# Kernel tuning notes

Hardware: AMD Instinct MI355X
Metric: run time of the kernel (lower is better)

## Reference

```python
import jax, jax.numpy as jnp
import numpy as np

B, S, D_MODEL = 2, 2048, 1024
NUM_HEADS = 16
D_HEAD = D_MODEL // NUM_HEADS
THETA = 10000.0


def setup_inputs() -> dict:
    key = jax.random.key(0)
    ks = jax.random.split(key, 5)
    std = float(np.sqrt(2.0 / (D_MODEL + D_MODEL)))
    return {
        "x": jax.random.normal(ks[0], (B, S, D_MODEL), dtype=jnp.float32),
        "wq": jax.random.normal(ks[1], (D_MODEL, D_MODEL), dtype=jnp.float32) * std,
        "wk": jax.random.normal(ks[2], (D_MODEL, D_MODEL), dtype=jnp.float32) * std,
        "wv": jax.random.normal(ks[3], (D_MODEL, D_MODEL), dtype=jnp.float32) * std,
        "wo": jax.random.normal(ks[4], (D_MODEL, D_MODEL), dtype=jnp.float32) * std,
    }


def _apply_rope(x):
    # x: [b, h, s, d]; interleaved even/odd RoPE rotation
    d = x.shape[-1]
    s = x.shape[-2]
    inv_freq = 1.0 / (THETA ** (jnp.arange(0, d, 2, dtype=x.dtype) / d))  # [d/2]
    pos = jnp.arange(s, dtype=x.dtype)
    freqs = pos[:, None] * inv_freq[None, :]  # [s, d/2]
    cos, sin = jnp.cos(freqs), jnp.sin(freqs)
    x_even = x[..., 0::2]
    x_odd = x[..., 1::2]
    rot_even = x_even * cos - x_odd * sin
    rot_odd = x_even * sin + x_odd * cos
    # interleave back: stack pairs on a new trailing axis then flatten
    return jnp.stack([rot_even, rot_odd], axis=-1).reshape(x.shape)


def reference(x, wq, wk, wv, wo):
    b, s, _ = x.shape
    # Linear applies weight [d_out, d_in] as x @ W^T
    q = jnp.einsum('bsd,ed->bse', x, wq)
    k = jnp.einsum('bsd,ed->bse', x, wk)
    v = jnp.einsum('bsd,ed->bse', x, wv)
    # [b, s, h*dh] -> [b, h, s, dh]
    q = q.reshape(b, s, NUM_HEADS, D_HEAD).transpose(0, 2, 1, 3)
    k = k.reshape(b, s, NUM_HEADS, D_HEAD).transpose(0, 2, 1, 3)
    v = v.reshape(b, s, NUM_HEADS, D_HEAD).transpose(0, 2, 1, 3)
    q = _apply_rope(q)
    k = _apply_rope(k)
    scores = jnp.einsum('bhqd,bhkd->bhqk', q, k) / jnp.sqrt(jnp.asarray(D_HEAD, x.dtype))
    causal = jnp.tril(jnp.ones((s, s), dtype=bool))  # allowed positions
    scores = jnp.where(causal, scores, -jnp.inf)
    attn = jax.nn.softmax(scores, axis=-1)
    out = jnp.einsum('bhqk,bhkd->bhqd', attn, v)
    out = out.transpose(0, 2, 1, 3).reshape(b, s, NUM_HEADS * D_HEAD)
    return jnp.einsum('bsd,ed->bse', out, wo)
```

## Files before the change

### kernel.cpp

```cpp
#include <hip/hip_runtime.h>
#include <stdint.h>

typedef unsigned short u16;
typedef __attribute__((ext_vector_type(8))) short bf16x8;
typedef __attribute__((ext_vector_type(4))) short bf16x4;
typedef __attribute__((ext_vector_type(4))) float f32x4;
typedef __attribute__((ext_vector_type(4))) unsigned short u16x4;
typedef __attribute__((ext_vector_type(2))) unsigned u32x2;

#define S_ 2048
#define E_ 1024
#define QSCALE 0.18033688011112042f

__device__ __forceinline__ u16 f2bf(float f) {
  union { float f; unsigned u; } v; v.f = f;
  unsigned u = v.u;
  unsigned r = (u + 0x7FFFu + ((u >> 16) & 1u)) >> 16;
  return (u16)r;
}
__device__ __forceinline__ float bf2f(u16 h) {
  union { unsigned u; float f; } v; v.u = ((unsigned)h) << 16;
  return v.f;
}
__device__ __forceinline__ unsigned cvtpk(float a, float b) {
  unsigned r;
  asm("v_cvt_pk_bf16_f32 %0, %1, %2" : "=v"(r) : "v"(a), "v"(b));
  return r;
}
__device__ __forceinline__ bf16x4 pk4(float a, float b, float c, float d) {
  union { u32x2 u; bf16x4 v; } U;
  U.u[0] = cvtpk(a, b);
  U.u[1] = cvtpk(c, d);
  return U.v;
}

typedef __attribute__((address_space(3))) void lds_void;
__device__ __forceinline__ unsigned lds_off(void* p) {
  return (unsigned)(unsigned long long)(lds_void*)p;
}
__device__ __forceinline__ void glds16(const u16* g, u16* l) {
  __builtin_amdgcn_global_load_lds(
      (const __attribute__((address_space(1))) void*)g,
      (__attribute__((address_space(3))) void*)l, 16, 0, 0);
}

__global__ void k_cast5(const float* __restrict__ x,
                        const float* __restrict__ wq, const float* __restrict__ wk,
                        const float* __restrict__ wv, const float* __restrict__ wo,
                        u16* __restrict__ xb, u16* __restrict__ wqb, u16* __restrict__ wkb,
                        u16* __restrict__ wvb, u16* __restrict__ wob) {
  int i = blockIdx.x * blockDim.x + threadIdx.x;
  const float* src; u16* dst; int off;
  if (i < 1048576) { src = x; dst = xb; off = i; }
  else {
    int j = i - 1048576;
    int w = j >> 18; off = j & 262143;
    src = (w == 0) ? wq : (w == 1) ? wk : (w == 2) ? wv : wo;
    dst = (w == 0) ? wqb : (w == 1) ? wkb : (w == 2) ? wvb : wob;
  }
  float4 v = *((const float4*)src + off);
  u16x4 o;
  o.x = f2bf(v.x); o.y = f2bf(v.y); o.z = f2bf(v.z); o.w = f2bf(v.w);
  *((u16x4*)dst + off) = o;
}

__global__ __launch_bounds__(256) void k_gemm(
    const u16* __restrict__ A,
    const u16* __restrict__ W0, const u16* __restrict__ W1, const u16* __restrict__ W2,
    void* O0, void* O1, void* O2, int outF32)
{
  __shared__ __align__(16) u16 As[2][128 * 32];
  __shared__ __align__(16) u16 Ws[2][128 * 32];
  int tid = threadIdx.x;
  int wid = tid >> 6, lane = tid & 63;
  int lg = lane >> 4, lr = lane & 15;
  int wsel = blockIdx.y >> 3, nb = blockIdx.y & 7;
  const u16* W = (wsel == 0) ? W0 : ((wsel == 1) ? W1 : W2);
  void* O = (wsel == 0) ? O0 : ((wsel == 1) ? O1 : O2);
  int m0 = blockIdx.x * 128;
  int n0 = nb * 128;
  int wr = wid >> 1, wc = wid & 1;

  f32x4 acc[4][4];
#pragma unroll
  for (int m = 0; m < 4; m++)
#pragma unroll
    for (int n = 0; n < 4; n++) acc[m][n] = (f32x4){0.f, 0.f, 0.f, 0.f};

  int srow = tid >> 2;
  int schunk = (tid & 3) ^ ((tid >> 3) & 3);
  const u16* ag = A + (size_t)(m0 + srow) * 1024 + schunk * 8;
  const u16* wg = W + (size_t)(n0 + srow) * 1024 + schunk * 8;

  int buf = 0;
  glds16(ag, &As[0][tid * 8]);
  glds16(ag + 65536, &As[0][tid * 8 + 2048]);
  glds16(wg, &Ws[0][tid * 8]);
  glds16(wg + 65536, &Ws[0][tid * 8 + 2048]);
  __syncthreads();

  for (int kt = 0; kt < 1024; kt += 32) {
    if (kt + 32 < 1024) {
      glds16(ag + kt + 32, &As[buf ^ 1][tid * 8]);
      glds16(ag + kt + 32 + 65536, &As[buf ^ 1][tid * 8 + 2048]);
      glds16(wg + kt + 32, &Ws[buf ^ 1][tid * 8]);
      glds16(wg + kt + 32 + 65536, &Ws[buf ^ 1][tid * 8 + 2048]);
    }
    bf16x8 af[4], wf[4];
#pragma unroll
    for (int m = 0; m < 4; m++) {
      int row = wr * 64 + m * 16 + lr;
      af[m] = *(const bf16x8*)&As[buf][row * 32 + ((lg ^ ((row >> 1) & 3)) * 8)];
    }
#pragma unroll
    for (int n = 0; n < 4; n++) {
      int row = wc * 64 + n * 16 + lr;
      wf[n] = *(const bf16x8*)&Ws[buf][row * 32 + ((lg ^ ((row >> 1) & 3)) * 8)];
    }
    __builtin_amdgcn_s_setprio(1);
#pragma unroll
    for (int m = 0; m < 4; m++)
#pragma unroll
      for (int n = 0; n < 4; n++)
        acc[m][n] = __builtin_amdgcn_mfma_f32_16x16x32_bf16(af[m], wf[n], acc[m][n], 0, 0, 0);
    __builtin_amdgcn_s_setprio(0);
    __syncthreads();
    buf ^= 1;
  }

#pragma unroll
  for (int m = 0; m < 4; m++) {
    int gr = m0 + wr * 64 + m * 16 + lg * 4;
#pragma unroll
    for (int n = 0; n < 4; n++) {
      int gc = n0 + wc * 64 + n * 16 + lr;
#pragma unroll
      for (int r = 0; r < 4; r++) {
        if (outF32) ((float*)O)[(size_t)(gr + r) * 1024 + gc] = acc[m][n][r];
        else ((u16*)O)[(size_t)(gr + r) * 1024 + gc] = f2bf(acc[m][n][r]);
      }
    }
  }
}

__global__ void k_rope(u16* __restrict__ Q, u16* __restrict__ K) {
  int idx = blockIdx.x * blockDim.x + threadIdx.x;
  int p = idx & 511;
  int srow = idx >> 9;
  int s = srow & (S_ - 1);
  int i = p & 31;
  float ang = (float)s * exp2f(-0.415241012f * (float)i);
  float sn, c;
  __sincosf(ang, &sn, &c);
  unsigned* qp = (unsigned*)Q + idx;
  unsigned qv = *qp;
  float e = bf2f((u16)(qv & 0xffff)), o = bf2f((u16)(qv >> 16));
  float re = (e * c - o * sn) * QSCALE, ro = (e * sn + o * c) * QSCALE;
  *qp = cvtpk(re, ro);
  unsigned* kp = (unsigned*)K + idx;
  unsigned kv = *kp;
  e = bf2f((u16)(kv & 0xffff)); o = bf2f((u16)(kv >> 16));
  re = e * c - o * sn; ro = e * sn + o * c;
  *kp = cvtpk(re, ro);
}

__global__ __launch_bounds__(256) void k_attn(
    const u16* __restrict__ Q, const u16* __restrict__ K,
    const u16* __restrict__ V, u16* __restrict__ AO)
{
  __shared__ __align__(16) u16 Ks[64 * 64];
  __shared__ __align__(16) u16 Vs[64 * 64];
  int tid = threadIdx.x;
  int wid = tid >> 6, lane = tid & 63;
  int lg = lane >> 4, lr = lane & 15;
  int bh = blockIdx.x;
  int qb = 31 - (int)blockIdx.y;
  int q0 = qb * 64 + wid * 16;
  size_t base = (size_t)(bh >> 4) * (2048u * 1024u) + (size_t)(bh & 15) * 64;

  const u16* qrow = Q + base + (size_t)(q0 + lr) * 1024 + lg * 8;
  bf16x8 qf0 = *(const bf16x8*)(qrow);
  bf16x8 qf1 = *(const bf16x8*)(qrow + 32);

  int srow = tid >> 3;
  int sch = tid & 7;
  const u16* kg = K + base + (size_t)srow * 1024 + sch * 8;
  const u16* vg = V + base + (size_t)srow * 1024 + sch * 8;
  int kwb0 = ((srow)*128 + sch * 16) ^ ((srow & 7) << 4);
  int kwb1 = ((srow + 32) * 128 + sch * 16) ^ ((srow & 7) << 4);
  int vwi0 = (srow >> 4) * 1024 + (sch >> 1) * 256 + (srow & 15) * 16 + (sch & 1) * 8;
  int vwi1 = ((srow + 32) >> 4) * 1024 + (sch >> 1) * 256 + (srow & 15) * 16 + (sch & 1) * 8;

  bf16x8 kr0 = *(const bf16x8*)(kg);
  bf16x8 kr1 = *(const bf16x8*)(kg + 32 * 1024);
  bf16x8 vr0 = *(const bf16x8*)(vg);
  bf16x8 vr1 = *(const bf16x8*)(vg + 32 * 1024);
  const u16* kgp = kg + 64 * 1024;
  const u16* vgp = vg + 64 * 1024;

  float m = -1e30f, lsum = 0.f;
  f32x4 o[4];
#pragma unroll
  for (int c = 0; c < 4; c++) o[c] = (f32x4){0.f, 0.f, 0.f, 0.f};

  int qg = q0 + lr;
  int ntile = qb + 1;
  unsigned vrd = lds_off(Vs) + (unsigned)(lane * 8);

  for (int t = 0; t < ntile; ++t) {
    __syncthreads();
    *(bf16x8*)((char*)Ks + kwb0) = kr0;
    *(bf16x8*)((char*)Ks + kwb1) = kr1;
    *(bf16x8*)(&Vs[vwi0]) = vr0;
    *(bf16x8*)(&Vs[vwi1]) = vr1;
    __syncthreads();
    if (t + 1 < ntile) {
      kr0 = *(const bf16x8*)(kgp);
      kr1 = *(const bf16x8*)(kgp + 32 * 1024);
      vr0 = *(const bf16x8*)(vgp);
      vr1 = *(const bf16x8*)(vgp + 32 * 1024);
      kgp += 64 * 1024;
      vgp += 64 * 1024;
    }
    f32x4 sv[4];
    int kv0 = t * 64;
    __builtin_amdgcn_s_setprio(1);
#pragma unroll
    for (int sub = 0; sub < 4; ++sub) {
      int row = sub * 16 + lr;
      int swz = (row & 7) << 4;
      bf16x8 kf0 = *(const bf16x8*)((const char*)Ks + ((row * 128 + lg * 16) ^ swz));
      bf16x8 kf1 = *(const bf16x8*)((const char*)Ks + ((row * 128 + 64 + lg * 16) ^ swz));
      f32x4 z = (f32x4){0.f, 0.f, 0.f, 0.f};
      z = __builtin_amdgcn_mfma_f32_16x16x32_bf16(kf0, qf0, z, 0, 0, 0);
      sv[sub] = __builtin_amdgcn_mfma_f32_16x16x32_bf16(kf1, qf1, z, 0, 0, 0);
    }
    __builtin_amdgcn_s_setprio(0);
    if (t == ntile - 1) {
#pragma unroll
      for (int sub = 0; sub < 4; ++sub)
#pragma unroll
        for (int j = 0; j < 4; ++j) {
          int kvg = kv0 + sub * 16 + lg * 4 + j;
          sv[sub][j] = (kvg <= qg) ? sv[sub][j] : -1e30f;
        }
    }
    float tm = fmaxf(fmaxf(fmaxf(sv[0][0], sv[0][1]), fmaxf(sv[0][2], sv[0][3])),
                     fmaxf(fmaxf(sv[1][0], sv[1][1]), fmaxf(sv[1][2], sv[1][3])));
    tm = fmaxf(tm, fmaxf(fmaxf(fmaxf(sv[2][0], sv[2][1]), fmaxf(sv[2][2], sv[2][3])),
                         fmaxf(fmaxf(sv[3][0], sv[3][1]), fmaxf(sv[3][2], sv[3][3]))));
    tm = fmaxf(tm, __shfl_xor(tm, 16));
    tm = fmaxf(tm, __shfl_xor(tm, 32));
    if (!__all(tm <= m + 8.f)) {
      float mn = fmaxf(m, tm);
      float corr = __builtin_amdgcn_exp2f(m - mn);
      m = mn;
      lsum *= corr;
#pragma unroll
      for (int c = 0; c < 4; ++c) {
        o[c][0] *= corr; o[c][1] *= corr; o[c][2] *= corr; o[c][3] *= corr;
      }
    }
    bf16x4 pb[4];
#pragma unroll
    for (int sub = 0; sub < 4; ++sub) {
      float p0 = __builtin_amdgcn_exp2f(sv[sub][0] - m);
      float p1 = __builtin_amdgcn_exp2f(sv[sub][1] - m);
      float p2 = __builtin_amdgcn_exp2f(sv[sub][2] - m);
      float p3 = __builtin_amdgcn_exp2f(sv[sub][3] - m);
      lsum += (p0 + p1) + (p2 + p3);
      pb[sub] = pk4(p0, p1, p2, p3);
    }
#pragma unroll
    for (int sub = 0; sub < 4; ++sub) {
      unsigned wa = vrd + (unsigned)(sub * 2048);
      bf16x4 va0, va1, va2, va3;
      asm volatile("ds_read_b64_tr_b16 %0, %1" : "=v"(va0) : "v"(wa));
      asm volatile("ds_read_b64_tr_b16 %0, %1 offset:512" : "=v"(va1) : "v"(wa));
      asm volatile("ds_read_b64_tr_b16 %0, %1 offset:1024" : "=v"(va2) : "v"(wa));
      asm volatile("ds_read_b64_tr_b16 %0, %1 offset:1536" : "=v"(va3) : "v"(wa));
      asm volatile("s_waitcnt lgkmcnt(0)" ::: "memory");
      __builtin_amdgcn_sched_barrier(0);
      __builtin_amdgcn_s_setprio(1);
      o[0] = __builtin_amdgcn_mfma_f32_16x16x16bf16_1k(va0, pb[sub], o[0], 0, 0, 0);
      o[1] = __builtin_amdgcn_mfma_f32_16x16x16bf16_1k(va1, pb[sub], o[1], 0, 0, 0);
      o[2] = __builtin_amdgcn_mfma_f32_16x16x16bf16_1k(va2, pb[sub], o[2], 0, 0, 0);
      o[3] = __builtin_amdgcn_mfma_f32_16x16x16bf16_1k(va3, pb[sub], o[3], 0, 0, 0);
      __builtin_amdgcn_s_setprio(0);
    }
  }

  float lt = lsum + __shfl_xor(lsum, 16);
  lt += __shfl_xor(lt, 32);
  float inv = 1.0f / lt;
  u16* orow = AO + base + (size_t)(q0 + lr) * 1024;
#pragma unroll
  for (int c = 0; c < 4; c++) {
    u32x2 pk;
    pk[0] = cvtpk(o[c][0] * inv, o[c][1] * inv);
    pk[1] = cvtpk(o[c][2] * inv, o[c][3] * inv);
    *(u32x2*)&orow[c * 16 + lg * 4] = pk;
  }
}

extern "C" void kernel_launch(void* const* d_in, const int* in_sizes, int n_in,
                              void* d_out, int out_size, void* d_ws, size_t ws_size,
                              hipStream_t stream) {
  const float* x = (const float*)d_in[0];
  const float* wq = (const float*)d_in[1];
  const float* wk = (const float*)d_in[2];
  const float* wv = (const float*)d_in[3];
  const float* wo = (const float*)d_in[4];

  char* ws = (char*)d_ws;
  u16* xb  = (u16*)(ws);
  u16* wqb = (u16*)(ws + 8388608);
  u16* wkb = (u16*)(ws + 10485760);
  u16* wvb = (u16*)(ws + 12582912);
  u16* wob = (u16*)(ws + 14680064);
  u16* Qb  = (u16*)(ws + 16777216);
  u16* Kb  = (u16*)(ws + 25165824);
  u16* Vb  = (u16*)(ws + 33554432);
  u16* AO  = (u16*)(ws + 41943040);

  k_cast5<<<8192, 256, 0, stream>>>(x, wq, wk, wv, wo, xb, wqb, wkb, wvb, wob);
  k_gemm<<<dim3(32, 24), 256, 0, stream>>>(xb, wqb, wkb, wvb, Qb, Kb, Vb, 0);
  k_rope<<<8192, 256, 0, stream>>>(Qb, Kb);
  k_attn<<<dim3(32, 32), 256, 0, stream>>>(Qb, Kb, Vb, AO);
  k_gemm<<<dim3(32, 8), 256, 0, stream>>>(AO, wob, wob, wob, d_out, d_out, d_out, 1);
}
```

Before: 115.7 us.

## Enlarge attention query block to 128 rows, two 16-row groups per wave

The attention kernel now processes 128 query rows per block, with each wave handling two 16-row query groups that share the same K/V tiles loaded into LDS. This halves the number of blocks and the K/V global loads and LDS staging per query, and reuses each K fragment and V transposed read for two MFMA chains. Waves whose causal range ends earlier skip the compute for later tiles but still take part in the loads and barriers, which adds some imbalance inside the block. It also doubles the accumulator register footprint, which may reduce occupancy, and there are fewer blocks (512) to spread across the CUs.

Measured after the change: 127.5 us. +10.2%, slower.

```diff
diff --git a/kernel.cpp b/kernel.cpp
--- a/kernel.cpp
+++ b/kernel.cpp
@@ -174,13 +174,15 @@
   int wid = tid >> 6, lane = tid & 63;
   int lg = lane >> 4, lr = lane & 15;
   int bh = blockIdx.x;
-  int qb = 31 - (int)blockIdx.y;
-  int q0 = qb * 64 + wid * 16;
+  int qb = 15 - (int)blockIdx.y;
+  int q0 = qb * 128 + wid * 32;
   size_t base = (size_t)(bh >> 4) * (2048u * 1024u) + (size_t)(bh & 15) * 64;
 
   const u16* qrow = Q + base + (size_t)(q0 + lr) * 1024 + lg * 8;
-  bf16x8 qf0 = *(const bf16x8*)(qrow);
-  bf16x8 qf1 = *(const bf16x8*)(qrow + 32);
+  bf16x8 qf0a = *(const bf16x8*)(qrow);
+  bf16x8 qf1a = *(const bf16x8*)(qrow + 32);
+  bf16x8 qf0b = *(const bf16x8*)(qrow + 16 * 1024);
+  bf16x8 qf1b = *(const bf16x8*)(qrow + 16 * 1024 + 32);
 
   int srow = tid >> 3;
   int sch = tid & 7;
@@ -198,23 +200,28 @@
   const u16* kgp = kg + 64 * 1024;
   const u16* vgp = vg + 64 * 1024;
 
-  float m = -1e30f, lsum = 0.f;
-  f32x4 o[4];
-#pragma unroll
-  for (int c = 0; c < 4; c++) o[c] = (f32x4){0.f, 0.f, 0.f, 0.f};
-
-  int qg = q0 + lr;
-  int ntile = qb + 1;
+  float ma = -1e30f, mb = -1e30f, lsa = 0.f, lsb = 0.f;
+  f32x4 oa[4], ob[4];
+#pragma unroll
+  for (int c = 0; c < 4; c++) {
+    oa[c] = (f32x4){0.f, 0.f, 0.f, 0.f};
+    ob[c] = (f32x4){0.f, 0.f, 0.f, 0.f};
+  }
+
+  int qga = q0 + lr;
+  int qgb = q0 + 16 + lr;
+  int ntw = (q0 >> 6) + 1;
+  int ntb = 2 * qb + 2;
   unsigned vrd = lds_off(Vs) + (unsigned)(lane * 8);
 
-  for (int t = 0; t < ntile; ++t) {
+  for (int t = 0; t < ntb; ++t) {
     __syncthreads();
     *(bf16x8*)((char*)Ks + kwb0) = kr0;
     *(bf16x8*)((char*)Ks + kwb1) = kr1;
     *(bf16x8*)(&Vs[vwi0]) = vr0;
     *(bf16x8*)(&Vs[vwi1]) = vr1;
     __syncthreads();
-    if (t + 1 < ntile) {
+    if (t + 1 < ntb) {
       kr0 = *(const bf16x8*)(kgp);
       kr1 = *(const bf16x8*)(kgp + 32 * 1024);
       vr0 = *(const bf16x8*)(vgp);
@@ -222,7 +229,9 @@
       kgp += 64 * 1024;
       vgp += 64 * 1024;
     }
-    f32x4 sv[4];
+    if (t >= ntw) continue;
+
+    f32x4 sa[4], sb[4];
     int kv0 = t * 64;
     __builtin_amdgcn_s_setprio(1);
 #pragma unroll
@@ -232,44 +241,62 @@
       bf16x8 kf0 = *(const bf16x8*)((const char*)Ks + ((row * 128 + lg * 16) ^ swz));
       bf16x8 kf1 = *(const bf16x8*)((const char*)Ks + ((row * 128 + 64 + lg * 16) ^ swz));
       f32x4 z = (f32x4){0.f, 0.f, 0.f, 0.f};
-      z = __builtin_amdgcn_mfma_f32_16x16x32_bf16(kf0, qf0, z, 0, 0, 0);
-      sv[sub] = __builtin_amdgcn_mfma_f32_16x16x32_bf16(kf1, qf1, z, 0, 0, 0);
+      z = __builtin_amdgcn_mfma_f32_16x16x32_bf16(kf0, qf0a, z, 0, 0, 0);
+      sa[sub] = __builtin_amdgcn_mfma_f32_16x16x32_bf16(kf1, qf1a, z, 0, 0, 0);
+      f32x4 z2 = (f32x4){0.f, 0.f, 0.f, 0.f};
+      z2 = __builtin_amdgcn_mfma_f32_16x16x32_bf16(kf0, qf0b, z2, 0, 0, 0);
+      sb[sub] = __builtin_amdgcn_mfma_f32_16x16x32_bf16(kf1, qf1b, z2, 0, 0, 0);
     }
     __builtin_amdgcn_s_setprio(0);
-    if (t == ntile - 1) {
+    if (t == ntw - 1) {
 #pragma unroll
       for (int sub = 0; sub < 4; ++sub)
 #pragma unroll
         for (int j = 0; j < 4; ++j) {
           int kvg = kv0 + sub * 16 + lg * 4 + j;
-          sv[sub][j] = (kvg <= qg) ? sv[sub][j] : -1e30f;
+          sa[sub][j] = (kvg <= qga) ? sa[sub][j] : -1e30f;
+          sb[sub][j] = (kvg <= qgb) ? sb[sub][j] : -1e30f;
         }
     }
-    float tm = fmaxf(fmaxf(fmaxf(sv[0][0], sv[0][1]), fmaxf(sv[0][2], sv[0][3])),
-                     fmaxf(fmaxf(sv[1][0], sv[1][1]), fmaxf(sv[1][2], sv[1][3])));
-    tm = fmaxf(tm, fmaxf(fmaxf(fmaxf(sv[2][0], sv[2][1]), fmaxf(sv[2][2], sv[2][3])),
-                         fmaxf(fmaxf(sv[3][0], sv[3][1]), fmaxf(sv[3][2], sv[3][3]))));
-    tm = fmaxf(tm, __shfl_xor(tm, 16));
-    tm = fmaxf(tm, __shfl_xor(tm, 32));
-    if (!__all(tm <= m + 8.f)) {
-      float mn = fmaxf(m, tm);
-      float corr = __builtin_amdgcn_exp2f(m - mn);
-      m = mn;
-      lsum *= corr;
+    float tma = fmaxf(fmaxf(fmaxf(sa[0][0], sa[0][1]), fmaxf(sa[0][2], sa[0][3])),
+                      fmaxf(fmaxf(sa[1][0], sa[1][1]), fmaxf(sa[1][2], sa[1][3])));
+    tma = fmaxf(tma, fmaxf(fmaxf(fmaxf(sa[2][0], sa[2][1]), fmaxf(sa[2][2], sa[2][3])),
+                           fmaxf(fmaxf(sa[3][0], sa[3][1]), fmaxf(sa[3][2], sa[3][3]))));
+    float tmb = fmaxf(fmaxf(fmaxf(sb[0][0], sb[0][1]), fmaxf(sb[0][2], sb[0][3])),
+                      fmaxf(fmaxf(sb[1][0], sb[1][1]), fmaxf(sb[1][2], sb[1][3])));
+    tmb = fmaxf(tmb, fmaxf(fmaxf(fmaxf(sb[2][0], sb[2][1]), fmaxf(sb[2][2], sb[2][3])),
+                           fmaxf(fmaxf(sb[3][0], sb[3][1]), fmaxf(sb[3][2], sb[3][3]))));
+    tma = fmaxf(tma, __shfl_xor(tma, 16));
+    tma = fmaxf(tma, __shfl_xor(tma, 32));
+    tmb = fmaxf(tmb, __shfl_xor(tmb, 16));
+    tmb = fmaxf(tmb, __shfl_xor(tmb, 32));
+    if (!__all((tma <= ma + 8.f) && (tmb <= mb + 8.f))) {
+      float mna = fmaxf(ma, tma), mnb = fmaxf(mb, tmb);
+      float ca = __builtin_amdgcn_exp2f(ma - mna);
+      float cb = __builtin_amdgcn_exp2f(mb - mnb);
+      ma = mna; mb = mnb;
+      lsa *= ca; lsb *= cb;
 #pragma unroll
       for (int c = 0; c < 4; ++c) {
-        o[c][0] *= corr; o[c][1] *= corr; o[c][2] *= corr; o[c][3] *= corr;
+        oa[c][0] *= ca; oa[c][1] *= ca; oa[c][2] *= ca; oa[c][3] *= ca;
+        ob[c][0] *= cb; ob[c][1] *= cb; ob[c][2] *= cb; ob[c][3] *= cb;
       }
     }
-    bf16x4 pb[4];
+    bf16x4 pa[4], pb[4];
 #pragma unroll
     for (int sub = 0; sub < 4; ++sub) {
-      float p0 = __builtin_amdgcn_exp2f(sv[sub][0] - m);
-      float p1 = __builtin_amdgcn_exp2f(sv[sub][1] - m);
-      float p2 = __builtin_amdgcn_exp2f(sv[sub][2] - m);
-      float p3 = __builtin_amdgcn_exp2f(sv[sub][3] - m);
-      lsum += (p0 + p1) + (p2 + p3);
-      pb[sub] = pk4(p0, p1, p2, p3);
+      float a0 = __builtin_amdgcn_exp2f(sa[sub][0] - ma);
+      float a1 = __builtin_amdgcn_exp2f(sa[sub][1] - ma);
+      float a2 = __builtin_amdgcn_exp2f(sa[sub][2] - ma);
+      float a3 = __builtin_amdgcn_exp2f(sa[sub][3] - ma);
+      lsa += (a0 + a1) + (a2 + a3);
+      pa[sub] = pk4(a0, a1, a2, a3);
+      float b0 = __builtin_amdgcn_exp2f(sb[sub][0] - mb);
+      float b1 = __builtin_amdgcn_exp2f(sb[sub][1] - mb);
+      float b2 = __builtin_amdgcn_exp2f(sb[sub][2] - mb);
+      float b3 = __builtin_amdgcn_exp2f(sb[sub][3] - mb);
+      lsb += (b0 + b1) + (b2 + b3);
+      pb[sub] = pk4(b0, b1, b2, b3);
     }
 #pragma unroll
     for (int sub = 0; sub < 4; ++sub) {
@@ -282,24 +309,35 @@
       asm volatile("s_waitcnt lgkmcnt(0)" ::: "memory");
       __builtin_amdgcn_sched_barrier(0);
       __builtin_amdgcn_s_setprio(1);
-      o[0] = __builtin_amdgcn_mfma_f32_16x16x16bf16_1k(va0, pb[sub], o[0], 0, 0, 0);
-      o[1] = __builtin_amdgcn_mfma_f32_16x16x16bf16_1k(va1, pb[sub], o[1], 0, 0, 0);
-      o[2] = __builtin_amdgcn_mfma_f32_16x16x16bf16_1k(va2, pb[sub], o[2], 0, 0, 0);
-      o[3] = __builtin_amdgcn_mfma_f32_16x16x16bf16_1k(va3, pb[sub], o[3], 0, 0, 0);
+      oa[0] = __builtin_amdgcn_mfma_f32_16x16x16bf16_1k(va0, pa[sub], oa[0], 0, 0, 0);
+      oa[1] = __builtin_amdgcn_mfma_f32_16x16x16bf16_1k(va1, pa[sub], oa[1], 0, 0, 0);
+      oa[2] = __builtin_amdgcn_mfma_f32_16x16x16bf16_1k(va2, pa[sub], oa[2], 0, 0, 0);
+      oa[3] = __builtin_amdgcn_mfma_f32_16x16x16bf16_1k(va3, pa[sub], oa[3], 0, 0, 0);
+      ob[0] = __builtin_amdgcn_mfma_f32_16x16x16bf16_1k(va0, pb[sub], ob[0], 0, 0, 0);
+      ob[1] = __builtin_amdgcn_mfma_f32_16x16x16bf16_1k(va1, pb[sub], ob[1], 0, 0, 0);
+      ob[2] = __builtin_amdgcn_mfma_f32_16x16x16bf16_1k(va2, pb[sub], ob[2], 0, 0, 0);
+      ob[3] = __builtin_amdgcn_mfma_f32_16x16x16bf16_1k(va3, pb[sub], ob[3], 0, 0, 0);
       __builtin_amdgcn_s_setprio(0);
     }
   }
 
-  float lt = lsum + __shfl_xor(lsum, 16);
-  lt += __shfl_xor(lt, 32);
-  float inv = 1.0f / lt;
-  u16* orow = AO + base + (size_t)(q0 + lr) * 1024;
+  float lta = lsa + __shfl_xor(lsa, 16);
+  lta += __shfl_xor(lta, 32);
+  float ltb = lsb + __shfl_xor(lsb, 16);
+  ltb += __shfl_xor(ltb, 32);
+  float inva = 1.0f / lta;
+  float invb = 1.0f / ltb;
+  u16* orowa = AO + base + (size_t)(q0 + lr) * 1024;
+  u16* orowb = orowa + 16 * 1024;
 #pragma unroll
   for (int c = 0; c < 4; c++) {
-    u32x2 pk;
-    pk[0] = cvtpk(o[c][0] * inv, o[c][1] * inv);
-    pk[1] = cvtpk(o[c][2] * inv, o[c][3] * inv);
-    *(u32x2*)&orow[c * 16 + lg * 4] = pk;
+    u32x2 pka, pkb;
+    pka[0] = cvtpk(oa[c][0] * inva, oa[c][1] * inva);
+    pka[1] = cvtpk(oa[c][2] * inva, oa[c][3] * inva);
+    *(u32x2*)&orowa[c * 16 + lg * 4] = pka;
+    pkb[0] = cvtpk(ob[c][0] * invb, ob[c][1] * invb);
+    pkb[1] = cvtpk(ob[c][2] * invb, ob[c][3] * invb);
+    *(u32x2*)&orowb[c * 16 + lg * 4] = pkb;
   }
 }
 
@@ -326,6 +364,6 @@
   k_cast5<<<8192, 256, 0, stream>>>(x, wq, wk, wv, wo, xb, wqb, wkb, wvb, wob);
   k_gemm<<<dim3(32, 24), 256, 0, stream>>>(xb, wqb, wkb, wvb, Qb, Kb, Vb, 0);
   k_rope<<<8192, 256, 0, stream>>>(Qb, Kb);
-  k_attn<<<dim3(32, 32), 256, 0, stream>>>(Qb, Kb, Vb, AO);
+  k_attn<<<dim3(32, 16), 256, 0, stream>>>(Qb, Kb, Vb, AO);
   k_gemm<<<dim3(32, 8), 256, 0, stream>>>(AO, wob, wob, wob, d_out, d_out, d_out, 1);
 }
```
